# Kernel optimization log

Measured on AMD Instinct MI355X. Metric: run time of the kernel, lower is better.

Reference implementation:

```python
import jax, jax.numpy as jnp
import numpy as np

N_HEADS = 4


def setup_inputs() -> dict:
    key = jax.random.key(0)
    ks = jax.random.split(key, 8)
    T, B, V, F = 30, 64, 32, 128   # len_pred, batch, n_vehicles, feature_size
    L, LF, TH = 64, 64, 20         # n_lanes, lane_feature_size, len_hist
    vehicles = jax.random.normal(ks[0], (T, B, V, F), dtype=jnp.float32)
    lanes = jax.random.normal(ks[1], (B, V, L, LF), dtype=jnp.float32)
    mask_lanes = jax.random.randint(ks[2], (TH, B, V, L), 0, 2).astype(bool)
    # torch Linear weight layout [out, in]; conv 1x1 weights squeezed to [out, in]
    Wk = jax.random.normal(ks[3], (F, LF), dtype=jnp.float32) / np.sqrt(LF)
    Wv = jax.random.normal(ks[4], (F, LF), dtype=jnp.float32) / np.sqrt(LF)
    Wq = jax.random.normal(ks[5], (F, F), dtype=jnp.float32) / np.sqrt(F)
    Wc = jax.random.normal(ks[6], (F, F), dtype=jnp.float32) / np.sqrt(F)
    return {"vehicles": vehicles, "lanes": lanes, "mask_lanes": mask_lanes,
            "Wk": Wk, "Wv": Wv, "Wq": Wq, "Wc": Wc}


def reference(vehicles, lanes, mask_lanes, Wk, Wv, Wq, Wc):
    # vehicles: [T,B,V,F], lanes: [B,V,L,LF], mask_lanes: [TH,B,V,L] bool
    T, B, V, F = vehicles.shape
    L = lanes.shape[2]
    H = N_HEADS
    hd = F // H
    # Linear projections of lanes (torch Linear: y = x @ W.T)
    k = jnp.einsum('bvlf,gf->bvlg', lanes, Wk).reshape(B, V, L, H, hd)
    v = jnp.einsum('bvlf,gf->bvlg', lanes, Wv).reshape(B, V, L, H, hd)
    # 1x1 Conv2d on feature channels == per-position linear
    q = jnp.einsum('tbvf,gf->tbvg', vehicles, Wq).reshape(T, B, V, H, hd)
    # mask: any over history dim -> [B,V,L] (the second any in attention is a no-op
    # since the mask is repeated identically over T and heads)
    mask = jnp.any(mask_lanes, axis=0)  # [B,V,L]
    scores = jnp.einsum('tbvhd,bvlhd->tbvhl', q, k) / jnp.sqrt(jnp.float32(hd))
    scores = jnp.where(mask[None, :, :, None, :], scores, jnp.float32(-1e9))
    p = jax.nn.softmax(scores, axis=-1)  # [T,B,V,H,L]
    out = jnp.einsum('tbvhl,bvlhd->tbvhd', p, v).reshape(T, B, V, F)
    out = jnp.einsum('tbvf,gf->tbvg', out, Wc) + vehicles
    return out
```

## Files before the change

kernel.cpp:

```cpp
#include <hip/hip_runtime.h>
#include <hip/hip_bf16.h>

#define T_  30
#define B_  64
#define V_  32
#define F_  128
#define L_  64
#define LF_ 64
#define TH_ 20
#define H_  4
#define HD_ 32

typedef __attribute__((ext_vector_type(8))) short bf16x8;
typedef __attribute__((ext_vector_type(4))) float f32x4;
#define MFMA(a,b,c) __builtin_amdgcn_mfma_f32_16x16x32_bf16(a, b, c, 0, 0, 0)

__device__ __forceinline__ float bf1(unsigned short u) {
    unsigned int x = ((unsigned int)u) << 16; float f; __builtin_memcpy(&f, &x, 4); return f;
}
__device__ __forceinline__ unsigned int cvtpk(float a, float b) {
    __hip_bfloat162 h = __float22bfloat162_rn(make_float2(a, b));
    unsigned int r; __builtin_memcpy(&r, &h, 4); return r;
}
__device__ __forceinline__ void st4pk(unsigned short* p, float a, float b, float c, float d) {
    uint2 u = { cvtpk(a, b), cvtpk(c, d) };
    *(uint2*)p = u;
}
__device__ __forceinline__ bf16x8 ldWfrag(const void* W, int off, bool isBf16) {
    if (isBf16) return *(const bf16x8*)((const unsigned short*)W + off);
    const float* p = (const float*)W + off;
    float4 a = *(const float4*)p;
    float4 b = *(const float4*)(p + 4);
    uint4 u = { cvtpk(a.x, a.y), cvtpk(a.z, a.w), cvtpk(b.x, b.y), cvtpk(b.z, b.w) };
    bf16x8 r; __builtin_memcpy(&r, &u, 16); return r;
}

__global__ __launch_bounds__(512, 4)
void lane_attn_kernel(const void* __restrict__ veh,
                      const void* __restrict__ lanes,
                      const void* __restrict__ maskp,
                      const void* __restrict__ Wk, const void* __restrict__ Wv,
                      const void* __restrict__ Wq, const void* __restrict__ Wc,
                      float* __restrict__ outp)
{
    const int bv    = blockIdx.x;
    const int tid   = threadIdx.x;
    const int w     = tid >> 6;
    const int h     = w >> 1;
    const int shalf = w & 1;
    const int lane  = tid & 63;
    const int quad  = lane >> 4;
    const int lm    = lane & 15;
    const int fbase = h * 32;
    const int fs    = fbase + shalf * 16;

    __shared__ __align__(16) unsigned short sRegion[14336];
    __shared__ __align__(16) unsigned short sK [64 * 136];
    __shared__ __align__(16) unsigned short sVt[128 * 72];
    unsigned short* sQ     = sRegion;
    unsigned short* sO     = sRegion;
    unsigned short* sLanes = sRegion + 4352;
    unsigned short* sVehB  = sRegion + 9984;
    unsigned short* sS     = sRegion + 4352;

    const unsigned short* vh16 = (const unsigned short*)veh;
    const int field = (vh16[2 * lane] >> 7) & 0xFF;
    const bool isBf16 = __popcll(__ballot(field >= 100 && field <= 130)) >= 32;
    const unsigned char* mbp = (const unsigned char*)maskp;
    const bool maskByte = (__ballot(mbp[4 * lane + 1] != 0) != 0ULL);

    bool ok;
    {
        const int* mi = (const int*)maskp;
        int o = 0;
        #pragma unroll
        for (int th = 0; th < TH_; ++th) {
            const size_t e = (size_t)th * (B_ * V_ * L_) + (size_t)bv * L_ + lane;
            o |= maskByte ? (int)mbp[e] : mi[e];
        }
        ok = (o != 0);
    }
    const unsigned long long mok = __ballot(ok);

    bf16x8 wbK[2], wbV[2], wq[4];
    #pragma unroll
    for (int kt = 0; kt < 2; ++kt) {
        const int off = (fs + lm) * 64 + kt * 32 + quad * 8;
        wbK[kt] = ldWfrag(Wk, off, isBf16);
        wbV[kt] = ldWfrag(Wv, off, isBf16);
    }
    #pragma unroll
    for (int kt = 0; kt < 4; ++kt)
        wq[kt] = ldWfrag(Wq, (fs + lm) * 128 + kt * 32 + quad * 8, isBf16);

    for (int u = tid; u < 64 * 16; u += 512) {
        const int l = u >> 4, c4 = u & 15;
        if (isBf16) {
            ushort4 x = ((const ushort4*)lanes)[bv * (L_ * LF_ / 4) + u];
            *(ushort4*)&sLanes[l * 88 + c4 * 4] = x;
        } else {
            float4 x = ((const float4*)lanes)[bv * (L_ * LF_ / 4) + u];
            uint2 y = { cvtpk(x.x, x.y), cvtpk(x.z, x.w) };
            *(uint2*)&sLanes[l * 88 + c4 * 4] = y;
        }
    }
    for (int u = tid; u < 32 * 32; u += 512) {
        const int t = u >> 5, c4 = u & 31;
        uint2 y = { 0, 0 };
        if (t < T_) {
            const int idx = (t * (B_ * V_) + bv) * (F_ / 4) + c4;
            if (isBf16) {
                ushort4 x = ((const ushort4*)veh)[idx];
                __builtin_memcpy(&y, &x, 8);
            } else {
                float4 x = ((const float4*)veh)[idx];
                y.x = cvtpk(x.x, x.y); y.y = cvtpk(x.z, x.w);
            }
        }
        *(uint2*)&sVehB[t * 136 + c4 * 4] = y;
    }
    __syncthreads();

    {
        f32x4 accK[4], accV[4];
        #pragma unroll
        for (int mt = 0; mt < 4; ++mt) { accK[mt] = (f32x4)0.f; accV[mt] = (f32x4)0.f; }
        #pragma unroll
        for (int kt = 0; kt < 2; ++kt) {
            bf16x8 a[4];
            #pragma unroll
            for (int mt = 0; mt < 4; ++mt)
                a[mt] = *(const bf16x8*)&sLanes[(mt * 16 + lm) * 88 + kt * 32 + quad * 8];
            #pragma unroll
            for (int mt = 0; mt < 4; ++mt) {
                accK[mt] = MFMA(wbK[kt], a[mt], accK[mt]);
                accV[mt] = MFMA(a[mt], wbV[kt], accV[mt]);
            }
        }
        #pragma unroll
        for (int mt = 0; mt < 4; ++mt) {
            st4pk(&sK[(mt * 16 + lm) * 136 + fs + quad * 4],
                  accK[mt][0], accK[mt][1], accK[mt][2], accK[mt][3]);
            st4pk(&sVt[(fs + lm) * 72 + mt * 16 + quad * 4],
                  accV[mt][0], accV[mt][1], accV[mt][2], accV[mt][3]);
        }
    }

    {
        f32x4 acc[2];
        acc[0] = (f32x4)0.f; acc[1] = (f32x4)0.f;
        #pragma unroll
        for (int kt = 0; kt < 4; ++kt) {
            bf16x8 b[2];
            #pragma unroll
            for (int nt = 0; nt < 2; ++nt)
                b[nt] = *(const bf16x8*)&sVehB[(nt * 16 + lm) * 136 + kt * 32 + quad * 8];
            #pragma unroll
            for (int nt = 0; nt < 2; ++nt) acc[nt] = MFMA(wq[kt], b[nt], acc[nt]);
        }
        const float sc = 0.17677669529663687f;
        #pragma unroll
        for (int nt = 0; nt < 2; ++nt)
            st4pk(&sQ[(nt * 16 + lm) * 136 + fs + quad * 4],
                  acc[nt][0] * sc, acc[nt][1] * sc, acc[nt][2] * sc, acc[nt][3] * sc);
    }

    bf16x8 wc[4];
    #pragma unroll
    for (int kt = 0; kt < 4; ++kt)
        wc[kt] = ldWfrag(Wc, (fs + lm) * 128 + kt * 32 + quad * 8, isBf16);

    __syncthreads();

    {
        bf16x8 a[4], b;
        #pragma unroll
        for (int mt = 0; mt < 4; ++mt)
            a[mt] = *(const bf16x8*)&sK[(mt * 16 + lm) * 136 + fbase + quad * 8];
        b = *(const bf16x8*)&sQ[(shalf * 16 + lm) * 136 + fbase + quad * 8];
        const int t = shalf * 16 + lm;
        const bool tok = (t < T_);
        const unsigned long long msh = (tok ? mok : 0ULL) >> (quad * 4);
        const unsigned int mlo = (unsigned int)msh, mhi = (unsigned int)(msh >> 32);
        #pragma unroll
        for (int mt = 0; mt < 4; ++mt) {
            f32x4 acc = MFMA(a[mt], b, (f32x4)0.f);
            const unsigned int mw = (mt >= 2) ? mhi : mlo;
            const int bp = (mt * 16) & 31;
            float e0 = ((mw >> (bp + 0)) & 1u) ? __expf(acc[0]) : 0.f;
            float e1 = ((mw >> (bp + 1)) & 1u) ? __expf(acc[1]) : 0.f;
            float e2 = ((mw >> (bp + 2)) & 1u) ? __expf(acc[2]) : 0.f;
            float e3 = ((mw >> (bp + 3)) & 1u) ? __expf(acc[3]) : 0.f;
            uint2 y = { cvtpk(e0, e1), cvtpk(e2, e3) };
            *(uint2*)&sS[(h * 32 + t) * 72 + mt * 16 + quad * 4] = y;
        }
    }

    {
        bf16x8 bones;
        #pragma unroll
        for (int j = 0; j < 8; ++j) bones[j] = (short)0x3F80;
        f32x4 acc[2], ssum;
        acc[0] = (f32x4)0.f; acc[1] = (f32x4)0.f; ssum = (f32x4)0.f;
        #pragma unroll
        for (int kt = 0; kt < 2; ++kt) {
            bf16x8 bp = *(const bf16x8*)&sS[(h * 32 + shalf * 16 + lm) * 72 + kt * 32 + quad * 8];
            bf16x8 av[2];
            #pragma unroll
            for (int mt = 0; mt < 2; ++mt)
                av[mt] = *(const bf16x8*)&sVt[(fbase + mt * 16 + lm) * 72 + kt * 32 + quad * 8];
            ssum = MFMA(bones, bp, ssum);
            #pragma unroll
            for (int mt = 0; mt < 2; ++mt) acc[mt] = MFMA(av[mt], bp, acc[mt]);
        }
        const float sv  = ssum[0];
        const float inv = (sv > 0.f) ? 1.f / sv : 0.f;
        const int t = shalf * 16 + lm;
        #pragma unroll
        for (int mt = 0; mt < 2; ++mt)
            st4pk(&sO[t * 136 + fbase + mt * 16 + quad * 4],
                  acc[mt][0] * inv, acc[mt][1] * inv, acc[mt][2] * inv, acc[mt][3] * inv);
    }

    float4 res[2];
    #pragma unroll
    for (int nt = 0; nt < 2; ++nt) {
        const int t = nt * 16 + lm;
        res[nt] = make_float4(0.f, 0.f, 0.f, 0.f);
        if (t < T_) {
            const size_t off = ((size_t)t * (B_ * V_) + bv) * F_ + fs + quad * 4;
            if (isBf16) {
                ushort4 u = *(const ushort4*)((const unsigned short*)veh + off);
                res[nt] = make_float4(bf1(u.x), bf1(u.y), bf1(u.z), bf1(u.w));
            } else {
                res[nt] = *(const float4*)((const float*)veh + off);
            }
        }
    }
    __syncthreads();

    {
        f32x4 acc[2];
        acc[0] = (f32x4)0.f; acc[1] = (f32x4)0.f;
        #pragma unroll
        for (int kt = 0; kt < 4; ++kt) {
            bf16x8 b[2];
            #pragma unroll
            for (int nt = 0; nt < 2; ++nt)
                b[nt] = *(const bf16x8*)&sO[(nt * 16 + lm) * 136 + kt * 32 + quad * 8];
            #pragma unroll
            for (int nt = 0; nt < 2; ++nt) acc[nt] = MFMA(wc[kt], b[nt], acc[nt]);
        }
        #pragma unroll
        for (int nt = 0; nt < 2; ++nt) {
            const int t = nt * 16 + lm;
            if (t < T_) {
                const size_t off = ((size_t)t * (B_ * V_) + bv) * F_ + fs + quad * 4;
                float4 o = make_float4(acc[nt][0] + res[nt].x, acc[nt][1] + res[nt].y,
                                       acc[nt][2] + res[nt].z, acc[nt][3] + res[nt].w);
                *(float4*)&outp[off] = o;
            }
        }
    }
}

extern "C" void kernel_launch(void* const* d_in, const int* in_sizes, int n_in,
                              void* d_out, int out_size, void* d_ws, size_t ws_size,
                              hipStream_t stream) {
    (void)in_sizes; (void)n_in; (void)out_size; (void)d_ws; (void)ws_size;
    lane_attn_kernel<<<dim3(B_ * V_), dim3(512), 0, stream>>>(
        d_in[0], d_in[1], d_in[2], d_in[3], d_in[4], d_in[5], d_in[6],
        (float*)d_out);
}
```

Measured before the change: 172.4 us.

## Restructure lane attention to keep K/V/Q/P in registers, one wave per head

```diff
diff --git a/kernel.cpp b/kernel.cpp
--- a/kernel.cpp
+++ b/kernel.cpp
@@ -11,9 +11,16 @@
 #define H_  4
 #define HD_ 32
 
-typedef __attribute__((ext_vector_type(8))) short bf16x8;
+typedef __attribute__((ext_vector_type(4))) short bf16x4;
 typedef __attribute__((ext_vector_type(4))) float f32x4;
-#define MFMA(a,b,c) __builtin_amdgcn_mfma_f32_16x16x32_bf16(a, b, c, 0, 0, 0)
+
+__device__ __forceinline__ f32x4 mfma16(bf16x4 a, bf16x4 b, f32x4 c) {
+#if defined(__HIP_DEVICE_COMPILE__)
+    return __builtin_amdgcn_mfma_f32_16x16x16bf16_1k(a, b, c, 0, 0, 0);
+#else
+    (void)a; (void)b; return c;
+#endif
+}
 
 __device__ __forceinline__ float bf1(unsigned short u) {
     unsigned int x = ((unsigned int)u) << 16; float f; __builtin_memcpy(&f, &x, 4); return f;
@@ -22,17 +29,21 @@
     __hip_bfloat162 h = __float22bfloat162_rn(make_float2(a, b));
     unsigned int r; __builtin_memcpy(&r, &h, 4); return r;
 }
-__device__ __forceinline__ void st4pk(unsigned short* p, float a, float b, float c, float d) {
-    uint2 u = { cvtpk(a, b), cvtpk(c, d) };
-    *(uint2*)p = u;
-}
-__device__ __forceinline__ bf16x8 ldWfrag(const void* W, int off, bool isBf16) {
-    if (isBf16) return *(const bf16x8*)((const unsigned short*)W + off);
-    const float* p = (const float*)W + off;
-    float4 a = *(const float4*)p;
-    float4 b = *(const float4*)(p + 4);
-    uint4 u = { cvtpk(a.x, a.y), cvtpk(a.z, a.w), cvtpk(b.x, b.y), cvtpk(b.z, b.w) };
-    bf16x8 r; __builtin_memcpy(&r, &u, 16); return r;
+__device__ __forceinline__ bf16x4 pk4(f32x4 v) {
+    uint2 u = { cvtpk(v[0], v[1]), cvtpk(v[2], v[3]) };
+    bf16x4 r; __builtin_memcpy(&r, &u, 8); return r;
+}
+__device__ __forceinline__ bf16x4 pk4s(f32x4 v, float s) {
+    uint2 u = { cvtpk(v[0] * s, v[1] * s), cvtpk(v[2] * s, v[3] * s) };
+    bf16x4 r; __builtin_memcpy(&r, &u, 8); return r;
+}
+__device__ __forceinline__ int swz128(int r, int c) { return r * 128 + (c ^ ((r & 7) << 3)); }
+__device__ __forceinline__ bf16x4 ldfrag(const void* M, int elemOff, bool isBf16) {
+    if (isBf16) return *(const bf16x4*)((const unsigned short*)M + elemOff);
+    const float* p = (const float*)M + elemOff;
+    float4 x = *(const float4*)p;
+    uint2 u = { cvtpk(x.x, x.y), cvtpk(x.z, x.w) };
+    bf16x4 r; __builtin_memcpy(&r, &u, 8); return r;
 }
 
 __global__ __launch_bounds__(512, 4)
@@ -43,25 +54,18 @@
                       const void* __restrict__ Wq, const void* __restrict__ Wc,
                       float* __restrict__ outp)
 {
-    const int bv    = blockIdx.x;
     const int tid   = threadIdx.x;
     const int w     = tid >> 6;
-    const int h     = w >> 1;
-    const int shalf = w & 1;
+    const int bvloc = w >> 2;
+    const int head  = w & 3;
+    const int bv    = blockIdx.x * 2 + bvloc;
     const int lane  = tid & 63;
     const int quad  = lane >> 4;
     const int lm    = lane & 15;
-    const int fbase = h * 32;
-    const int fs    = fbase + shalf * 16;
-
-    __shared__ __align__(16) unsigned short sRegion[14336];
-    __shared__ __align__(16) unsigned short sK [64 * 136];
-    __shared__ __align__(16) unsigned short sVt[128 * 72];
-    unsigned short* sQ     = sRegion;
-    unsigned short* sO     = sRegion;
-    unsigned short* sLanes = sRegion + 4352;
-    unsigned short* sVehB  = sRegion + 9984;
-    unsigned short* sS     = sRegion + 4352;
+    const int q4    = quad * 4;
+    const int fbase = head * 32;
+
+    __shared__ __align__(16) unsigned short sO[2][4096];
 
     const unsigned short* vh16 = (const unsigned short*)veh;
     const int field = (vh16[2 * lane] >> 7) & 0xFF;
@@ -82,185 +86,157 @@
     }
     const unsigned long long mok = __ballot(ok);
 
-    bf16x8 wbK[2], wbV[2], wq[4];
+    const void* lanesBV = isBf16
+        ? (const void*)((const unsigned short*)lanes + (size_t)bv * (L_ * LF_))
+        : (const void*)((const float*)lanes + (size_t)bv * (L_ * LF_));
+
+    bf16x4 KB[2][4], VA[4][2];
+    {
+        f32x4 accK[2][4], accV[4][2];
+        #pragma unroll
+        for (int ft = 0; ft < 2; ++ft)
+            #pragma unroll
+            for (int lt = 0; lt < 4; ++lt) { accK[ft][lt] = (f32x4)0.f; accV[lt][ft] = (f32x4)0.f; }
+        #pragma unroll
+        for (int ct = 0; ct < 4; ++ct) {
+            bf16x4 wk[2], wv[2], lb[4];
+            #pragma unroll
+            for (int ft = 0; ft < 2; ++ft) {
+                wk[ft] = ldfrag(Wk, (fbase + ft * 16 + lm) * 64 + ct * 16 + q4, isBf16);
+                wv[ft] = ldfrag(Wv, (fbase + ft * 16 + lm) * 64 + ct * 16 + q4, isBf16);
+            }
+            #pragma unroll
+            for (int lt = 0; lt < 4; ++lt)
+                lb[lt] = ldfrag(lanesBV, (lt * 16 + lm) * 64 + ct * 16 + q4, isBf16);
+            #pragma unroll
+            for (int ft = 0; ft < 2; ++ft)
+                #pragma unroll
+                for (int lt = 0; lt < 4; ++lt) {
+                    accK[ft][lt] = mfma16(wk[ft], lb[lt], accK[ft][lt]);
+                    accV[lt][ft] = mfma16(lb[lt], wv[ft], accV[lt][ft]);
+                }
+        }
+        #pragma unroll
+        for (int ft = 0; ft < 2; ++ft)
+            #pragma unroll
+            for (int lt = 0; lt < 4; ++lt) { KB[ft][lt] = pk4(accK[ft][lt]); VA[lt][ft] = pk4(accV[lt][ft]); }
+    }
+
+    bf16x4 QB[2][2];
+    {
+        f32x4 accQ[2][2];
+        accQ[0][0] = (f32x4)0.f; accQ[0][1] = (f32x4)0.f;
+        accQ[1][0] = (f32x4)0.f; accQ[1][1] = (f32x4)0.f;
+        #pragma unroll
+        for (int kt = 0; kt < 8; ++kt) {
+            bf16x4 wq[2], vb[2];
+            #pragma unroll
+            for (int gt = 0; gt < 2; ++gt)
+                wq[gt] = ldfrag(Wq, (fbase + gt * 16 + lm) * 128 + kt * 16 + q4, isBf16);
+            #pragma unroll
+            for (int tt = 0; tt < 2; ++tt) {
+                const int t = tt * 16 + lm;
+                bf16x4 z = { 0, 0, 0, 0 };
+                vb[tt] = (t < T_)
+                    ? ldfrag(veh, (int)(((size_t)t * (B_ * V_) + bv) * F_) + kt * 16 + q4, isBf16)
+                    : z;
+            }
+            #pragma unroll
+            for (int gt = 0; gt < 2; ++gt)
+                #pragma unroll
+                for (int tt = 0; tt < 2; ++tt) accQ[gt][tt] = mfma16(wq[gt], vb[tt], accQ[gt][tt]);
+        }
+        const float sc = 0.17677669529663687f;
+        #pragma unroll
+        for (int gt = 0; gt < 2; ++gt)
+            #pragma unroll
+            for (int tt = 0; tt < 2; ++tt) QB[gt][tt] = pk4s(accQ[gt][tt], sc);
+    }
+
+    bf16x4 PB[4][2];
+    float inv[2];
+    {
+        float psum[2] = { 0.f, 0.f };
+        #pragma unroll
+        for (int lt = 0; lt < 4; ++lt) {
+            const unsigned int m4 = (unsigned int)((mok >> (lt * 16 + q4)) & 0xFULL);
+            #pragma unroll
+            for (int tt = 0; tt < 2; ++tt) {
+                f32x4 s = (f32x4)0.f;
+                #pragma unroll
+                for (int ft = 0; ft < 2; ++ft) s = mfma16(KB[ft][lt], QB[ft][tt], s);
+                const bool tok = (tt * 16 + lm) < T_;
+                float e0 = (tok && (m4 & 1u)) ? __expf(s[0]) : 0.f;
+                float e1 = (tok && (m4 & 2u)) ? __expf(s[1]) : 0.f;
+                float e2 = (tok && (m4 & 4u)) ? __expf(s[2]) : 0.f;
+                float e3 = (tok && (m4 & 8u)) ? __expf(s[3]) : 0.f;
+                psum[tt] += (e0 + e1) + (e2 + e3);
+                uint2 u = { cvtpk(e0, e1), cvtpk(e2, e3) };
+                __builtin_memcpy(&PB[lt][tt], &u, 8);
+            }
+        }
+        #pragma unroll
+        for (int tt = 0; tt < 2; ++tt) {
+            float p = psum[tt];
+            p += __shfl_xor(p, 16, 64);
+            p += __shfl_xor(p, 32, 64);
+            inv[tt] = (p > 0.f) ? 1.f / p : 0.f;
+        }
+    }
+
     #pragma unroll
-    for (int kt = 0; kt < 2; ++kt) {
-        const int off = (fs + lm) * 64 + kt * 32 + quad * 8;
-        wbK[kt] = ldWfrag(Wk, off, isBf16);
-        wbV[kt] = ldWfrag(Wv, off, isBf16);
-    }
-    #pragma unroll
-    for (int kt = 0; kt < 4; ++kt)
-        wq[kt] = ldWfrag(Wq, (fs + lm) * 128 + kt * 32 + quad * 8, isBf16);
-
-    for (int u = tid; u < 64 * 16; u += 512) {
-        const int l = u >> 4, c4 = u & 15;
-        if (isBf16) {
-            ushort4 x = ((const ushort4*)lanes)[bv * (L_ * LF_ / 4) + u];
-            *(ushort4*)&sLanes[l * 88 + c4 * 4] = x;
-        } else {
-            float4 x = ((const float4*)lanes)[bv * (L_ * LF_ / 4) + u];
-            uint2 y = { cvtpk(x.x, x.y), cvtpk(x.z, x.w) };
-            *(uint2*)&sLanes[l * 88 + c4 * 4] = y;
-        }
-    }
-    for (int u = tid; u < 32 * 32; u += 512) {
-        const int t = u >> 5, c4 = u & 31;
-        uint2 y = { 0, 0 };
-        if (t < T_) {
-            const int idx = (t * (B_ * V_) + bv) * (F_ / 4) + c4;
-            if (isBf16) {
-                ushort4 x = ((const ushort4*)veh)[idx];
-                __builtin_memcpy(&y, &x, 8);
-            } else {
-                float4 x = ((const float4*)veh)[idx];
-                y.x = cvtpk(x.x, x.y); y.y = cvtpk(x.z, x.w);
-            }
-        }
-        *(uint2*)&sVehB[t * 136 + c4 * 4] = y;
-    }
+    for (int ft = 0; ft < 2; ++ft)
+        #pragma unroll
+        for (int tt = 0; tt < 2; ++tt) {
+            f32x4 o = (f32x4)0.f;
+            #pragma unroll
+            for (int lt = 0; lt < 4; ++lt) o = mfma16(VA[lt][ft], PB[lt][tt], o);
+            uint2 u = { cvtpk(o[0] * inv[tt], o[1] * inv[tt]),
+                        cvtpk(o[2] * inv[tt], o[3] * inv[tt]) };
+            *(uint2*)&sO[bvloc][swz128(tt * 16 + lm, fbase + ft * 16 + q4)] = u;
+        }
+
     __syncthreads();
 
     {
-        f32x4 accK[4], accV[4];
-        #pragma unroll
-        for (int mt = 0; mt < 4; ++mt) { accK[mt] = (f32x4)0.f; accV[mt] = (f32x4)0.f; }
-        #pragma unroll
-        for (int kt = 0; kt < 2; ++kt) {
-            bf16x8 a[4];
-            #pragma unroll
-            for (int mt = 0; mt < 4; ++mt)
-                a[mt] = *(const bf16x8*)&sLanes[(mt * 16 + lm) * 88 + kt * 32 + quad * 8];
-            #pragma unroll
-            for (int mt = 0; mt < 4; ++mt) {
-                accK[mt] = MFMA(wbK[kt], a[mt], accK[mt]);
-                accV[mt] = MFMA(a[mt], wbV[kt], accV[mt]);
-            }
-        }
-        #pragma unroll
-        for (int mt = 0; mt < 4; ++mt) {
-            st4pk(&sK[(mt * 16 + lm) * 136 + fs + quad * 4],
-                  accK[mt][0], accK[mt][1], accK[mt][2], accK[mt][3]);
-            st4pk(&sVt[(fs + lm) * 72 + mt * 16 + quad * 4],
-                  accV[mt][0], accV[mt][1], accV[mt][2], accV[mt][3]);
-        }
-    }
-
-    {
-        f32x4 acc[2];
-        acc[0] = (f32x4)0.f; acc[1] = (f32x4)0.f;
-        #pragma unroll
-        for (int kt = 0; kt < 4; ++kt) {
-            bf16x8 b[2];
-            #pragma unroll
-            for (int nt = 0; nt < 2; ++nt)
-                b[nt] = *(const bf16x8*)&sVehB[(nt * 16 + lm) * 136 + kt * 32 + quad * 8];
-            #pragma unroll
-            for (int nt = 0; nt < 2; ++nt) acc[nt] = MFMA(wq[kt], b[nt], acc[nt]);
-        }
-        const float sc = 0.17677669529663687f;
-        #pragma unroll
-        for (int nt = 0; nt < 2; ++nt)
-            st4pk(&sQ[(nt * 16 + lm) * 136 + fs + quad * 4],
-                  acc[nt][0] * sc, acc[nt][1] * sc, acc[nt][2] * sc, acc[nt][3] * sc);
-    }
-
-    bf16x8 wc[4];
-    #pragma unroll
-    for (int kt = 0; kt < 4; ++kt)
-        wc[kt] = ldWfrag(Wc, (fs + lm) * 128 + kt * 32 + quad * 8, isBf16);
-
-    __syncthreads();
-
-    {
-        bf16x8 a[4], b;
-        #pragma unroll
-        for (int mt = 0; mt < 4; ++mt)
-            a[mt] = *(const bf16x8*)&sK[(mt * 16 + lm) * 136 + fbase + quad * 8];
-        b = *(const bf16x8*)&sQ[(shalf * 16 + lm) * 136 + fbase + quad * 8];
-        const int t = shalf * 16 + lm;
-        const bool tok = (t < T_);
-        const unsigned long long msh = (tok ? mok : 0ULL) >> (quad * 4);
-        const unsigned int mlo = (unsigned int)msh, mhi = (unsigned int)(msh >> 32);
-        #pragma unroll
-        for (int mt = 0; mt < 4; ++mt) {
-            f32x4 acc = MFMA(a[mt], b, (f32x4)0.f);
-            const unsigned int mw = (mt >= 2) ? mhi : mlo;
-            const int bp = (mt * 16) & 31;
-            float e0 = ((mw >> (bp + 0)) & 1u) ? __expf(acc[0]) : 0.f;
-            float e1 = ((mw >> (bp + 1)) & 1u) ? __expf(acc[1]) : 0.f;
-            float e2 = ((mw >> (bp + 2)) & 1u) ? __expf(acc[2]) : 0.f;
-            float e3 = ((mw >> (bp + 3)) & 1u) ? __expf(acc[3]) : 0.f;
-            uint2 y = { cvtpk(e0, e1), cvtpk(e2, e3) };
-            *(uint2*)&sS[(h * 32 + t) * 72 + mt * 16 + quad * 4] = y;
-        }
-    }
-
-    {
-        bf16x8 bones;
-        #pragma unroll
-        for (int j = 0; j < 8; ++j) bones[j] = (short)0x3F80;
-        f32x4 acc[2], ssum;
-        acc[0] = (f32x4)0.f; acc[1] = (f32x4)0.f; ssum = (f32x4)0.f;
-        #pragma unroll
-        for (int kt = 0; kt < 2; ++kt) {
-            bf16x8 bp = *(const bf16x8*)&sS[(h * 32 + shalf * 16 + lm) * 72 + kt * 32 + quad * 8];
-            bf16x8 av[2];
-            #pragma unroll
-            for (int mt = 0; mt < 2; ++mt)
-                av[mt] = *(const bf16x8*)&sVt[(fbase + mt * 16 + lm) * 72 + kt * 32 + quad * 8];
-            ssum = MFMA(bones, bp, ssum);
-            #pragma unroll
-            for (int mt = 0; mt < 2; ++mt) acc[mt] = MFMA(av[mt], bp, acc[mt]);
-        }
-        const float sv  = ssum[0];
-        const float inv = (sv > 0.f) ? 1.f / sv : 0.f;
-        const int t = shalf * 16 + lm;
-        #pragma unroll
-        for (int mt = 0; mt < 2; ++mt)
-            st4pk(&sO[t * 136 + fbase + mt * 16 + quad * 4],
-                  acc[mt][0] * inv, acc[mt][1] * inv, acc[mt][2] * inv, acc[mt][3] * inv);
-    }
-
-    float4 res[2];
-    #pragma unroll
-    for (int nt = 0; nt < 2; ++nt) {
-        const int t = nt * 16 + lm;
-        res[nt] = make_float4(0.f, 0.f, 0.f, 0.f);
-        if (t < T_) {
-            const size_t off = ((size_t)t * (B_ * V_) + bv) * F_ + fs + quad * 4;
-            if (isBf16) {
-                ushort4 u = *(const ushort4*)((const unsigned short*)veh + off);
-                res[nt] = make_float4(bf1(u.x), bf1(u.y), bf1(u.z), bf1(u.w));
-            } else {
-                res[nt] = *(const float4*)((const float*)veh + off);
-            }
-        }
-    }
-    __syncthreads();
-
-    {
-        f32x4 acc[2];
-        acc[0] = (f32x4)0.f; acc[1] = (f32x4)0.f;
-        #pragma unroll
-        for (int kt = 0; kt < 4; ++kt) {
-            bf16x8 b[2];
-            #pragma unroll
-            for (int nt = 0; nt < 2; ++nt)
-                b[nt] = *(const bf16x8*)&sO[(nt * 16 + lm) * 136 + kt * 32 + quad * 8];
-            #pragma unroll
-            for (int nt = 0; nt < 2; ++nt) acc[nt] = MFMA(wc[kt], b[nt], acc[nt]);
-        }
-        #pragma unroll
-        for (int nt = 0; nt < 2; ++nt) {
-            const int t = nt * 16 + lm;
-            if (t < T_) {
-                const size_t off = ((size_t)t * (B_ * V_) + bv) * F_ + fs + quad * 4;
-                float4 o = make_float4(acc[nt][0] + res[nt].x, acc[nt][1] + res[nt].y,
-                                       acc[nt][2] + res[nt].z, acc[nt][3] + res[nt].w);
-                *(float4*)&outp[off] = o;
-            }
-        }
+        f32x4 acc[2][2];
+        acc[0][0] = (f32x4)0.f; acc[0][1] = (f32x4)0.f;
+        acc[1][0] = (f32x4)0.f; acc[1][1] = (f32x4)0.f;
+        #pragma unroll
+        for (int kt = 0; kt < 8; ++kt) {
+            bf16x4 wc[2], ob[2];
+            #pragma unroll
+            for (int gt = 0; gt < 2; ++gt)
+                wc[gt] = ldfrag(Wc, (fbase + gt * 16 + lm) * 128 + kt * 16 + q4, isBf16);
+            #pragma unroll
+            for (int tt = 0; tt < 2; ++tt) {
+                uint2 u = *(const uint2*)&sO[bvloc][swz128(tt * 16 + lm, kt * 16 + q4)];
+                __builtin_memcpy(&ob[tt], &u, 8);
+            }
+            #pragma unroll
+            for (int gt = 0; gt < 2; ++gt)
+                #pragma unroll
+                for (int tt = 0; tt < 2; ++tt) acc[gt][tt] = mfma16(wc[gt], ob[tt], acc[gt][tt]);
+        }
+        #pragma unroll
+        for (int gt = 0; gt < 2; ++gt)
+            #pragma unroll
+            for (int tt = 0; tt < 2; ++tt) {
+                const int t = tt * 16 + lm;
+                if (t < T_) {
+                    const size_t off = ((size_t)t * (B_ * V_) + bv) * F_ + fbase + gt * 16 + q4;
+                    float4 r;
+                    if (isBf16) {
+                        ushort4 u = *(const ushort4*)((const unsigned short*)veh + off);
+                        r = make_float4(bf1(u.x), bf1(u.y), bf1(u.z), bf1(u.w));
+                    } else {
+                        r = *(const float4*)((const float*)veh + off);
+                    }
+                    float4 o = make_float4(acc[gt][tt][0] + r.x, acc[gt][tt][1] + r.y,
+                                           acc[gt][tt][2] + r.z, acc[gt][tt][3] + r.w);
+                    *(float4*)&outp[off] = o;
+                }
+            }
     }
 }
 
@@ -268,7 +244,7 @@
                               void* d_out, int out_size, void* d_ws, size_t ws_size,
                               hipStream_t stream) {
     (void)in_sizes; (void)n_in; (void)out_size; (void)d_ws; (void)ws_size;
-    lane_attn_kernel<<<dim3(B_ * V_), dim3(512), 0, stream>>>(
+    lane_attn_kernel<<<dim3(B_ * V_ / 2), dim3(512), 0, stream>>>(
         d_in[0], d_in[1], d_in[2], d_in[3], d_in[4], d_in[5], d_in[6],
         (float*)d_out);
 }
```

Result: slower. 222.6 us (+29.1%).
